# Optimization experiments

Hardware: AMD Instinct MI355X
Metric: run time of the kernel (lower is better)

Reference implementation:

```python
import jax, jax.numpy as jnp
import numpy as np
from jax import lax

B, h, Ch = 16, 8, 32
HW = 56
N = HW * HW
SPLITS = [64, 96, 96]  # [2*Ch, 3*Ch, 3*Ch] for windows {3,5,7}


def _dwconv(x, w, b, pad):
    # x: [B, C, H, W]; w: [C, 1, k, k] depthwise (feature_group_count=C)
    y = lax.conv_general_dilated(
        x, w, window_strides=(1, 1), padding=[(pad, pad), (pad, pad)],
        feature_group_count=x.shape[1],
        dimension_numbers=('NCHW', 'OIHW', 'NCHW'))
    return y + b[None, :, None, None]


def setup_inputs() -> dict:
    key = jax.random.key(0)
    ks = jax.random.split(key, 6)
    return {
        'q': jax.random.normal(ks[0], (B, h, N, Ch), dtype=jnp.float32),
        'v': jax.random.normal(ks[1], (B, h, N, Ch), dtype=jnp.float32),
        'w3': jax.random.normal(ks[2], (64, 1, 3, 3), dtype=jnp.float32) * 0.1,
        'b3': jnp.zeros((64,), dtype=jnp.float32),
        'w5': jax.random.normal(ks[3], (96, 1, 5, 5), dtype=jnp.float32) * 0.1,
        'b5': jnp.zeros((96,), dtype=jnp.float32),
        'w7': jax.random.normal(ks[4], (96, 1, 7, 7), dtype=jnp.float32) * 0.1,
        'b7': jnp.zeros((96,), dtype=jnp.float32),
        'H': HW,
        'W': HW,
    }


def reference(q, v, w3, b3, w5, b5, w7, b7, H, W):
    # q, v: [B, h, N, Ch]; N == H*W, Nv == N (same-resolution path, no interpolation)
    Bq, hh, Nq, C = q.shape
    # v: B h (H W) Ch -> B (h*Ch) H W
    v_img = jnp.transpose(v, (0, 1, 3, 2)).reshape(Bq, hh * C, H, W)
    v1, v2, v3 = jnp.split(v_img, np.cumsum(SPLITS)[:-1], axis=1)
    conv_v = jnp.concatenate([
        _dwconv(v1, w3, b3, 1),
        _dwconv(v2, w5, b5, 2),
        _dwconv(v3, w7, b7, 3),
    ], axis=1)  # [B, h*Ch, H, W]
    # B (h*Ch) H W -> B h (H W) Ch
    conv_v = conv_v.reshape(Bq, hh, C, H * W).transpose(0, 1, 3, 2)
    ev = q * conv_v  # [B, h, N, Ch]
    # transpose(1,2).flatten(2): [B, N, h*Ch]
    return jnp.transpose(ev, (0, 2, 1, 3)).reshape(Bq, Nq, hh * C)
```

## Files before the change

### kernel.cpp

```cpp
#include <hip/hip_runtime.h>
#include <cstddef>


#define BH 16
#define NH 8
#define CH 32
#define HW 56
#define NN (HW*HW)
#define ROWB (HW*CH*4)
#define BUF_PX 72
#define BUF_FLOATS (BUF_PX*CH)

typedef float f32x4 __attribute__((ext_vector_type(4)));
typedef unsigned int u32x4 __attribute__((ext_vector_type(4)));

__device__ __forceinline__ f32x4 bload(__amdgpu_buffer_rsrc_t rs, int voff) {
    u32x4 u = __builtin_amdgcn_raw_buffer_load_b128(rs, voff, 0, 0);
    f32x4 f; __builtin_memcpy(&f, &u, 16); return f;
}

template<int K>
__device__ __forceinline__ void run_head(
    const float* __restrict__ q, const float* __restrict__ v,
    const float* __restrict__ w, const float* __restrict__ bias,
    float* __restrict__ out, int b, int hh, int y0, int cbase,
    float* __restrict__ w_lds, float* __restrict__ bufs)
{
    constexpr int P = K / 2;
    constexpr int NR = 7 + K - 1;
    const int t = threadIdx.x;

    const int nw = K * K * CH;
    for (int i = t; i < nw; i += 256) {
        int tap = i >> 5, c = i & 31;
        w_lds[tap * CH + c] = w[(cbase + c) * (K * K) + tap];
    }
    __syncthreads();

    const int wid  = t >> 6;
    const int lane = t & 63;
    float* wb = bufs + wid * BUF_FLOATS;

    {
        f32x4 z = {0.f, 0.f, 0.f, 0.f};
        *(f32x4*)(wb + lane * 4) = z;
        *(f32x4*)(wb + 64 * CH + lane * 4) = z;
    }

    const int y    = y0 + wid;
    const int xseg = lane >> 3;
    const int chq  = lane & 7;
    const int x0   = xseg * 7;
    const int ch   = chq * 4;

    const size_t plane = ((size_t)b * NH + hh) * (size_t)NN * CH;
    const float* vb   = v + plane;
    const float* qrow = q + plane + (size_t)y * (HW * CH);

    f32x4 bias4 = *(const f32x4*)(bias + cbase + ch);
    f32x4 acc[7];
#pragma unroll
    for (int i = 0; i < 7; ++i) acc[i] = bias4;

#pragma unroll
    for (int dy = 0; dy < K; ++dy) {
        const int yy = y + dy - P;
        const bool ok = (unsigned)yy < (unsigned)HW;
        const float* base = vb + (ptrdiff_t)yy * (HW * CH);
        __amdgpu_buffer_rsrc_t rs = __builtin_amdgcn_make_buffer_rsrc(
            (void*)base, (short)0, ok ? ROWB : 0, 0x00020000);

        f32x4 ld[7];
#pragma unroll
        for (int k = 0; k < 7; ++k) ld[k] = bload(rs, k * 1024 + lane * 16);
#pragma unroll
        for (int k = 0; k < 7; ++k)
            *(f32x4*)(wb + (k + 1) * 256 + lane * 4) = ld[k];

        f32x4 r[NR];
        const float* rb = wb + (size_t)(x0 - P + 8) * CH + ch;
#pragma unroll
        for (int j = 0; j < NR; ++j)
            r[j] = *(const f32x4*)(rb + j * CH);

#pragma unroll
        for (int dx = 0; dx < K; ++dx) {
            const f32x4 w4 = *(const f32x4*)(w_lds + (dy * K + dx) * CH + ch);
#pragma unroll
            for (int i = 0; i < 7; ++i)
                acc[i] += r[i + dx] * w4;
        }
    }

#pragma unroll
    for (int i = 0; i < 7; ++i)
        *(f32x4*)(wb + (size_t)(x0 + i + 8) * CH + ch) = acc[i];

    float* orow = out + ((size_t)b * NN + (size_t)y * HW) * (NH * CH) + hh * CH;
    const int px_l = lane >> 3;
    const int chl  = (lane & 7) * 4;
#pragma unroll
    for (int k = 0; k < 7; ++k) {
        const f32x4 c4 = *(const f32x4*)(wb + (size_t)(k * 8 + px_l + 8) * CH + chl);
        const f32x4 q4 = *(const f32x4*)(qrow + k * 256 + lane * 4);
        const f32x4 o  = c4 * q4;
        *(f32x4*)(orow + (size_t)(k * 8 + px_l) * (NH * CH) + chl) = o;
    }
}

__global__ __launch_bounds__(256, 3)
void clusterformer_fused(const float* __restrict__ q, const float* __restrict__ v,
                         const float* __restrict__ w3, const float* __restrict__ b3,
                         const float* __restrict__ w5, const float* __restrict__ b5,
                         const float* __restrict__ w7, const float* __restrict__ b7,
                         float* __restrict__ out)
{
    __shared__ __align__(16) float bufs[4 * BUF_FLOATS];
    __shared__ __align__(16) float w_lds[49 * CH];

    const int bid  = blockIdx.x;
    const int p_lo = bid & 7;
    const int t2   = bid >> 3;
    const int p_hi = t2 / 14;
    const int yg   = t2 % 14;
    const int p    = p_hi * 8 + p_lo;
    const int b    = p & 15;
    const int hhp  = p >> 4;
    const int hh   = (hhp < 3) ? (5 + hhp) : ((hhp < 6) ? (hhp - 1) : (hhp - 6));
    const int y0   = yg * 4;

    if (hh < 2)      run_head<3>(q, v, w3, b3, out, b, hh, y0, hh * 32,       w_lds, bufs);
    else if (hh < 5) run_head<5>(q, v, w5, b5, out, b, hh, y0, hh * 32 - 64,  w_lds, bufs);
    else             run_head<7>(q, v, w7, b7, out, b, hh, y0, hh * 32 - 160, w_lds, bufs);
}

extern "C" void kernel_launch(void* const* d_in, const int* in_sizes, int n_in,
                              void* d_out, int out_size, void* d_ws, size_t ws_size,
                              hipStream_t stream) {
    const float* q  = (const float*)d_in[0];
    const float* v  = (const float*)d_in[1];
    const float* w3 = (const float*)d_in[2];
    const float* b3 = (const float*)d_in[3];
    const float* w5 = (const float*)d_in[4];
    const float* b5 = (const float*)d_in[5];
    const float* w7 = (const float*)d_in[6];
    const float* b7 = (const float*)d_in[7];
    float* out = (float*)d_out;

    const int grid = BH * NH * 14;
    clusterformer_fused<<<grid, 256, 0, stream>>>(q, v, w3, b3, w5, b5, w7, b7, out);
}
```

Baseline: 164.4 us.

## Load halo pixels directly from global via buffer loads, drop LDS staging

Instead of staging each input row through a per-wave LDS buffer and reading the shifted windows back out, each lane now issues buffer loads straight from global memory for all NR window pixels. Out-of-range columns get an out-of-bounds offset so the buffer hardware returns zeros. The output is written directly from registers rather than being transposed through LDS, and the occupancy hint rises from 3 to 4 blocks. This removes LDS traffic and frees LDS for occupancy, but issues more global loads (about NR/7 times as many, overlapping across lanes) and leaves the output stores less coalesced.

```diff
diff --git a/kernel.cpp b/kernel.cpp
--- a/kernel.cpp
+++ b/kernel.cpp
@@ -8,8 +8,6 @@
 #define HW 56
 #define NN (HW*HW)
 #define ROWB (HW*CH*4)
-#define BUF_PX 72
-#define BUF_FLOATS (BUF_PX*CH)
 
 typedef float f32x4 __attribute__((ext_vector_type(4)));
 typedef unsigned int u32x4 __attribute__((ext_vector_type(4)));
@@ -24,7 +22,7 @@
     const float* __restrict__ q, const float* __restrict__ v,
     const float* __restrict__ w, const float* __restrict__ bias,
     float* __restrict__ out, int b, int hh, int y0, int cbase,
-    float* __restrict__ w_lds, float* __restrict__ bufs)
+    float* __restrict__ w_lds)
 {
     constexpr int P = K / 2;
     constexpr int NR = 7 + K - 1;
@@ -39,14 +37,6 @@
 
     const int wid  = t >> 6;
     const int lane = t & 63;
-    float* wb = bufs + wid * BUF_FLOATS;
-
-    {
-        f32x4 z = {0.f, 0.f, 0.f, 0.f};
-        *(f32x4*)(wb + lane * 4) = z;
-        *(f32x4*)(wb + 64 * CH + lane * 4) = z;
-    }
-
     const int y    = y0 + wid;
     const int xseg = lane >> 3;
     const int chq  = lane & 7;
@@ -57,7 +47,14 @@
     const float* vb   = v + plane;
     const float* qrow = q + plane + (size_t)y * (HW * CH);
 
-    f32x4 bias4 = *(const f32x4*)(bias + cbase + ch);
+    int vx[NR];
+#pragma unroll
+    for (int j = 0; j < NR; ++j) {
+        const int px = x0 - P + j;
+        vx[j] = ((unsigned)px < (unsigned)HW) ? (px * CH + ch) * 4 : 0x40000000;
+    }
+
+    const f32x4 bias4 = *(const f32x4*)(bias + cbase + ch);
     f32x4 acc[7];
 #pragma unroll
     for (int i = 0; i < 7; ++i) acc[i] = bias4;
@@ -70,18 +67,9 @@
         __amdgpu_buffer_rsrc_t rs = __builtin_amdgcn_make_buffer_rsrc(
             (void*)base, (short)0, ok ? ROWB : 0, 0x00020000);
 
-        f32x4 ld[7];
+        f32x4 r[NR];
 #pragma unroll
-        for (int k = 0; k < 7; ++k) ld[k] = bload(rs, k * 1024 + lane * 16);
-#pragma unroll
-        for (int k = 0; k < 7; ++k)
-            *(f32x4*)(wb + (k + 1) * 256 + lane * 4) = ld[k];
-
-        f32x4 r[NR];
-        const float* rb = wb + (size_t)(x0 - P + 8) * CH + ch;
-#pragma unroll
-        for (int j = 0; j < NR; ++j)
-            r[j] = *(const f32x4*)(rb + j * CH);
+        for (int j = 0; j < NR; ++j) r[j] = bload(rs, vx[j]);
 
 #pragma unroll
         for (int dx = 0; dx < K; ++dx) {
@@ -92,30 +80,22 @@
         }
     }
 
+    float* obase = out + ((size_t)b * NN + (size_t)y * HW) * (NH * CH) + hh * CH + ch;
 #pragma unroll
-    for (int i = 0; i < 7; ++i)
-        *(f32x4*)(wb + (size_t)(x0 + i + 8) * CH + ch) = acc[i];
-
-    float* orow = out + ((size_t)b * NN + (size_t)y * HW) * (NH * CH) + hh * CH;
-    const int px_l = lane >> 3;
-    const int chl  = (lane & 7) * 4;
-#pragma unroll
-    for (int k = 0; k < 7; ++k) {
-        const f32x4 c4 = *(const f32x4*)(wb + (size_t)(k * 8 + px_l + 8) * CH + chl);
-        const f32x4 q4 = *(const f32x4*)(qrow + k * 256 + lane * 4);
-        const f32x4 o  = c4 * q4;
-        *(f32x4*)(orow + (size_t)(k * 8 + px_l) * (NH * CH) + chl) = o;
+    for (int i = 0; i < 7; ++i) {
+        const int px = x0 + i;
+        const f32x4 q4 = *(const f32x4*)(qrow + (size_t)px * CH + ch);
+        *(f32x4*)(obase + (size_t)px * (NH * CH)) = acc[i] * q4;
     }
 }
 
-__global__ __launch_bounds__(256, 3)
+__global__ __launch_bounds__(256, 4)
 void clusterformer_fused(const float* __restrict__ q, const float* __restrict__ v,
                          const float* __restrict__ w3, const float* __restrict__ b3,
                          const float* __restrict__ w5, const float* __restrict__ b5,
                          const float* __restrict__ w7, const float* __restrict__ b7,
                          float* __restrict__ out)
 {
-    __shared__ __align__(16) float bufs[4 * BUF_FLOATS];
     __shared__ __align__(16) float w_lds[49 * CH];
 
     const int bid  = blockIdx.x;
@@ -129,9 +109,9 @@
     const int hh   = (hhp < 3) ? (5 + hhp) : ((hhp < 6) ? (hhp - 1) : (hhp - 6));
     const int y0   = yg * 4;
 
-    if (hh < 2)      run_head<3>(q, v, w3, b3, out, b, hh, y0, hh * 32,       w_lds, bufs);
-    else if (hh < 5) run_head<5>(q, v, w5, b5, out, b, hh, y0, hh * 32 - 64,  w_lds, bufs);
-    else             run_head<7>(q, v, w7, b7, out, b, hh, y0, hh * 32 - 160, w_lds, bufs);
+    if (hh < 2)      run_head<3>(q, v, w3, b3, out, b, hh, y0, hh * 32,       w_lds);
+    else if (hh < 5) run_head<5>(q, v, w5, b5, out, b, hh, y0, hh * 32 - 64,  w_lds);
+    else             run_head<7>(q, v, w7, b7, out, b, hh, y0, hh * 32 - 160, w_lds);
 }
 
 extern "C" void kernel_launch(void* const* d_in, const int* in_sizes, int n_in,
```

New measurement: 167.6 us. No clear change (+2.0%).

## Share staged input row halo across waves in LDS instead of per-wave reloads

Applied to the files above, without the earlier changes.

The four waves of a block now cooperatively load the 4+2P input rows once into a single shared LDS tile with zero-padded borders. Previously each wave reloaded its own K rows from global memory, which duplicated traffic across the overlapping row halos. Q is preloaded into registers so the output is written directly, dropping the LDS round-trip used for the transpose. The cost is a larger LDS footprint, so launch bounds fall from 3 to 2 blocks per SM, and a block-wide barrier is added.

```diff
diff --git a/kernel.cpp b/kernel.cpp
--- a/kernel.cpp
+++ b/kernel.cpp
@@ -8,7 +8,8 @@
 #define HW 56
 #define NN (HW*HW)
 #define ROWB (HW*CH*4)
-#define BUF_PX 72
+#define RS 58
+#define BUF_PX 584
 #define BUF_FLOATS (BUF_PX*CH)
 
 typedef float f32x4 __attribute__((ext_vector_type(4)));
@@ -28,6 +29,7 @@
 {
     constexpr int P = K / 2;
     constexpr int NR = 7 + K - 1;
+    constexpr int NROWS = 4 + 2 * P;
     const int t = threadIdx.x;
 
     const int nw = K * K * CH;
@@ -35,18 +37,24 @@
         int tap = i >> 5, c = i & 31;
         w_lds[tap * CH + c] = w[(cbase + c) * (K * K) + tap];
     }
-    __syncthreads();
+
+    {
+        f32x4 z = {0.f, 0.f, 0.f, 0.f};
+        const int NG = P + 2 * NROWS + 1;
+        if (t < NG * 8) {
+            const int g = t >> 3, sub = t & 7;
+            int px;
+            if (g < P) px = g;
+            else if (g < P + 2 * NROWS) {
+                const int rr = (g - P) >> 1;
+                px = P + rr * RS + 56 + ((g - P) & 1);
+            } else px = P + NROWS * RS;
+            *(f32x4*)(bufs + px * CH + sub * 4) = z;
+        }
+    }
 
     const int wid  = t >> 6;
     const int lane = t & 63;
-    float* wb = bufs + wid * BUF_FLOATS;
-
-    {
-        f32x4 z = {0.f, 0.f, 0.f, 0.f};
-        *(f32x4*)(wb + lane * 4) = z;
-        *(f32x4*)(wb + 64 * CH + lane * 4) = z;
-    }
-
     const int y    = y0 + wid;
     const int xseg = lane >> 3;
     const int chq  = lane & 7;
@@ -57,31 +65,43 @@
     const float* vb   = v + plane;
     const float* qrow = q + plane + (size_t)y * (HW * CH);
 
-    f32x4 bias4 = *(const f32x4*)(bias + cbase + ch);
+    f32x4 qf[7];
+#pragma unroll
+    for (int i = 0; i < 7; ++i)
+        qf[i] = *(const f32x4*)(qrow + (size_t)(x0 + i) * CH + ch);
+
+    for (int rr = wid; rr < NROWS; rr += 4) {
+        const int yy = y0 - P + rr;
+        const bool ok = (unsigned)yy < (unsigned)HW;
+        __amdgpu_buffer_rsrc_t rs = __builtin_amdgcn_make_buffer_rsrc(
+            (void*)(vb + (ptrdiff_t)yy * (HW * CH)), (short)0, ok ? ROWB : 0, 0x00020000);
+        f32x4 ld[7];
+#pragma unroll
+        for (int k = 0; k < 7; ++k) ld[k] = bload(rs, k * 1024 + lane * 16);
+        float* dst = bufs + (size_t)(P + rr * RS) * CH;
+#pragma unroll
+        for (int k = 0; k < 7; ++k)
+            *(f32x4*)(dst + k * 256 + lane * 4) = ld[k];
+    }
+    __syncthreads();
+
+    const float mL = (xseg == 0) ? 0.f : 1.f;
+    const float mR = (xseg == 7) ? 0.f : 1.f;
+
+    const f32x4 bias4 = *(const f32x4*)(bias + cbase + ch);
     f32x4 acc[7];
 #pragma unroll
     for (int i = 0; i < 7; ++i) acc[i] = bias4;
 
 #pragma unroll
     for (int dy = 0; dy < K; ++dy) {
-        const int yy = y + dy - P;
-        const bool ok = (unsigned)yy < (unsigned)HW;
-        const float* base = vb + (ptrdiff_t)yy * (HW * CH);
-        __amdgpu_buffer_rsrc_t rs = __builtin_amdgcn_make_buffer_rsrc(
-            (void*)base, (short)0, ok ? ROWB : 0, 0x00020000);
-
-        f32x4 ld[7];
-#pragma unroll
-        for (int k = 0; k < 7; ++k) ld[k] = bload(rs, k * 1024 + lane * 16);
-#pragma unroll
-        for (int k = 0; k < 7; ++k)
-            *(f32x4*)(wb + (k + 1) * 256 + lane * 4) = ld[k];
-
+        const int rr = wid + dy;
+        const float* rb = bufs + (size_t)(rr * RS + x0) * CH + ch;
         f32x4 r[NR];
-        const float* rb = wb + (size_t)(x0 - P + 8) * CH + ch;
 #pragma unroll
         for (int j = 0; j < NR; ++j)
             r[j] = *(const f32x4*)(rb + j * CH);
+        if constexpr (K == 7) { r[0] *= mL; r[NR - 1] *= mR; }
 
 #pragma unroll
         for (int dx = 0; dx < K; ++dx) {
@@ -92,30 +112,20 @@
         }
     }
 
+    float* obase = out + ((size_t)b * NN + (size_t)y * HW) * (NH * CH) + hh * CH + ch;
 #pragma unroll
     for (int i = 0; i < 7; ++i)
-        *(f32x4*)(wb + (size_t)(x0 + i + 8) * CH + ch) = acc[i];
-
-    float* orow = out + ((size_t)b * NN + (size_t)y * HW) * (NH * CH) + hh * CH;
-    const int px_l = lane >> 3;
-    const int chl  = (lane & 7) * 4;
-#pragma unroll
-    for (int k = 0; k < 7; ++k) {
-        const f32x4 c4 = *(const f32x4*)(wb + (size_t)(k * 8 + px_l + 8) * CH + chl);
-        const f32x4 q4 = *(const f32x4*)(qrow + k * 256 + lane * 4);
-        const f32x4 o  = c4 * q4;
-        *(f32x4*)(orow + (size_t)(k * 8 + px_l) * (NH * CH) + chl) = o;
-    }
+        *(f32x4*)(obase + (size_t)(x0 + i) * (NH * CH)) = acc[i] * qf[i];
 }
 
-__global__ __launch_bounds__(256, 3)
+__global__ __launch_bounds__(256, 2)
 void clusterformer_fused(const float* __restrict__ q, const float* __restrict__ v,
                          const float* __restrict__ w3, const float* __restrict__ b3,
                          const float* __restrict__ w5, const float* __restrict__ b5,
                          const float* __restrict__ w7, const float* __restrict__ b7,
                          float* __restrict__ out)
 {
-    __shared__ __align__(16) float bufs[4 * BUF_FLOATS];
+    __shared__ __align__(16) float bufs[BUF_FLOATS];
     __shared__ __align__(16) float w_lds[49 * CH];
 
     const int bid  = blockIdx.x;
```

Result: no change. 161.8 us (-1.6%).

## Assign one output row across all heads per block and stage full-row output in LDS

Applied to the files above, without the earlier changes.

Each block now handles one (batch, row) pair across all 8 heads, with each wave processing two heads. Weights for all three kernel sizes are loaded into LDS once per block, and results are staged in an LDS row buffer so the global output write covers the full 256-channel row contiguously. The change also prefetches the next v row while the current one is processed (double-buffered registers) and loads q into registers early. The cost is a much larger LDS footprint (about 96KB) with launch bounds lowered to one block per CU, a grid of only 896 blocks, and unequal per-wave work, since waves pair 3x3, 5x5 and 7x7 heads differently.

```diff
diff --git a/kernel.cpp b/kernel.cpp
--- a/kernel.cpp
+++ b/kernel.cpp
@@ -8,8 +8,12 @@
 #define HW 56
 #define NN (HW*HW)
 #define ROWB (HW*CH*4)
-#define BUF_PX 72
-#define BUF_FLOATS (BUF_PX*CH)
+#define WBF 2304
+#define OUTROWF 264
+#define W3O 0
+#define W5O 576
+#define W7O 2976
+#define WTOT 7680
 
 typedef float f32x4 __attribute__((ext_vector_type(4)));
 typedef unsigned int u32x4 __attribute__((ext_vector_type(4)));
@@ -19,35 +23,16 @@
     f32x4 f; __builtin_memcpy(&f, &u, 16); return f;
 }
 
-template<int K>
-__device__ __forceinline__ void run_head(
+template<int K, int CT>
+__device__ __forceinline__ void head_row(
     const float* __restrict__ q, const float* __restrict__ v,
-    const float* __restrict__ w, const float* __restrict__ bias,
-    float* __restrict__ out, int b, int hh, int y0, int cbase,
-    float* __restrict__ w_lds, float* __restrict__ bufs)
+    const float* __restrict__ whead,
+    const float* __restrict__ bias_g,
+    float* __restrict__ outL, float* __restrict__ wb,
+    int b, int hh, int cbase, int y, int lane)
 {
-    constexpr int P = K / 2;
+    constexpr int P  = K / 2;
     constexpr int NR = 7 + K - 1;
-    const int t = threadIdx.x;
-
-    const int nw = K * K * CH;
-    for (int i = t; i < nw; i += 256) {
-        int tap = i >> 5, c = i & 31;
-        w_lds[tap * CH + c] = w[(cbase + c) * (K * K) + tap];
-    }
-    __syncthreads();
-
-    const int wid  = t >> 6;
-    const int lane = t & 63;
-    float* wb = bufs + wid * BUF_FLOATS;
-
-    {
-        f32x4 z = {0.f, 0.f, 0.f, 0.f};
-        *(f32x4*)(wb + lane * 4) = z;
-        *(f32x4*)(wb + 64 * CH + lane * 4) = z;
-    }
-
-    const int y    = y0 + wid;
     const int xseg = lane >> 3;
     const int chq  = lane & 7;
     const int x0   = xseg * 7;
@@ -56,36 +41,50 @@
     const size_t plane = ((size_t)b * NH + hh) * (size_t)NN * CH;
     const float* vb   = v + plane;
     const float* qrow = q + plane + (size_t)y * (HW * CH);
+    const float* whc  = whead + cbase + ch;
 
-    f32x4 bias4 = *(const f32x4*)(bias + cbase + ch);
+    f32x4 qf[7];
+#pragma unroll
+    for (int i = 0; i < 7; ++i)
+        qf[i] = *(const f32x4*)(qrow + (size_t)(x0 + i) * CH + ch);
+
+    const f32x4 bias4 = *(const f32x4*)(bias_g + ch);
     f32x4 acc[7];
 #pragma unroll
     for (int i = 0; i < 7; ++i) acc[i] = bias4;
 
+    f32x4 ld[2][7];
+    {
+        const int yy = y - P;
+        const bool ok = (unsigned)yy < (unsigned)HW;
+        __amdgpu_buffer_rsrc_t rs0 = __builtin_amdgcn_make_buffer_rsrc(
+            (void*)(vb + (ptrdiff_t)yy * (HW * CH)), (short)0, ok ? ROWB : 0, 0x00020000);
+#pragma unroll
+        for (int k = 0; k < 7; ++k) ld[0][k] = bload(rs0, k * 1024 + lane * 16);
+    }
 #pragma unroll
     for (int dy = 0; dy < K; ++dy) {
-        const int yy = y + dy - P;
-        const bool ok = (unsigned)yy < (unsigned)HW;
-        const float* base = vb + (ptrdiff_t)yy * (HW * CH);
-        __amdgpu_buffer_rsrc_t rs = __builtin_amdgcn_make_buffer_rsrc(
-            (void*)base, (short)0, ok ? ROWB : 0, 0x00020000);
-
-        f32x4 ld[7];
+        if (dy + 1 < K) {
+            const int yy = y + dy + 1 - P;
+            const bool ok = (unsigned)yy < (unsigned)HW;
+            __amdgpu_buffer_rsrc_t rs = __builtin_amdgcn_make_buffer_rsrc(
+                (void*)(vb + (ptrdiff_t)yy * (HW * CH)), (short)0, ok ? ROWB : 0, 0x00020000);
 #pragma unroll
-        for (int k = 0; k < 7; ++k) ld[k] = bload(rs, k * 1024 + lane * 16);
+            for (int k = 0; k < 7; ++k) ld[(dy + 1) & 1][k] = bload(rs, k * 1024 + lane * 16);
+        }
 #pragma unroll
         for (int k = 0; k < 7; ++k)
-            *(f32x4*)(wb + (k + 1) * 256 + lane * 4) = ld[k];
+            *(f32x4*)(wb + (k + 1) * 256 + lane * 4) = ld[dy & 1][k];
 
+        const float* rb = wb + (size_t)(x0 - P + 8) * CH + ch;
         f32x4 r[NR];
-        const float* rb = wb + (size_t)(x0 - P + 8) * CH + ch;
 #pragma unroll
         for (int j = 0; j < NR; ++j)
             r[j] = *(const f32x4*)(rb + j * CH);
 
 #pragma unroll
         for (int dx = 0; dx < K; ++dx) {
-            const f32x4 w4 = *(const f32x4*)(w_lds + (dy * K + dx) * CH + ch);
+            const f32x4 w4 = *(const f32x4*)(whc + (dy * K + dx) * CT);
 #pragma unroll
             for (int i = 0; i < 7; ++i)
                 acc[i] += r[i + dx] * w4;
@@ -94,44 +93,81 @@
 
 #pragma unroll
     for (int i = 0; i < 7; ++i)
-        *(f32x4*)(wb + (size_t)(x0 + i + 8) * CH + ch) = acc[i];
-
-    float* orow = out + ((size_t)b * NN + (size_t)y * HW) * (NH * CH) + hh * CH;
-    const int px_l = lane >> 3;
-    const int chl  = (lane & 7) * 4;
-#pragma unroll
-    for (int k = 0; k < 7; ++k) {
-        const f32x4 c4 = *(const f32x4*)(wb + (size_t)(k * 8 + px_l + 8) * CH + chl);
-        const f32x4 q4 = *(const f32x4*)(qrow + k * 256 + lane * 4);
-        const f32x4 o  = c4 * q4;
-        *(f32x4*)(orow + (size_t)(k * 8 + px_l) * (NH * CH) + chl) = o;
-    }
+        *(f32x4*)(outL + (size_t)(x0 + i) * OUTROWF + hh * CH + ch) = acc[i] * qf[i];
 }
 
-__global__ __launch_bounds__(256, 3)
+__device__ __forceinline__ void do_head(
+    const float* q, const float* v,
+    const float* w_lds,
+    const float* b3, const float* b5, const float* b7,
+    float* outL, float* wb, int b, int hh, int y, int lane)
+{
+    if (hh < 2)
+        head_row<3, 64>(q, v, w_lds + W3O, b3 + hh * 32,        outL, wb, b, hh, hh * 32,       y, lane);
+    else if (hh < 5)
+        head_row<5, 96>(q, v, w_lds + W5O, b5 + hh * 32 - 64,   outL, wb, b, hh, hh * 32 - 64,  y, lane);
+    else
+        head_row<7, 96>(q, v, w_lds + W7O, b7 + hh * 32 - 160,  outL, wb, b, hh, hh * 32 - 160, y, lane);
+}
+
+__global__ __launch_bounds__(256, 1)
 void clusterformer_fused(const float* __restrict__ q, const float* __restrict__ v,
                          const float* __restrict__ w3, const float* __restrict__ b3,
                          const float* __restrict__ w5, const float* __restrict__ b5,
                          const float* __restrict__ w7, const float* __restrict__ b7,
                          float* __restrict__ out)
 {
-    __shared__ __align__(16) float bufs[4 * BUF_FLOATS];
-    __shared__ __align__(16) float w_lds[49 * CH];
+    __shared__ __align__(16) float w_lds[WTOT];
+    __shared__ __align__(16) float bufs[4 * WBF];
+    __shared__ __align__(16) float outL[HW * OUTROWF];
+
+    const int t    = threadIdx.x;
+    const int wid  = t >> 6;
+    const int lane = t & 63;
 
     const int bid  = blockIdx.x;
-    const int p_lo = bid & 7;
-    const int t2   = bid >> 3;
-    const int p_hi = t2 / 14;
-    const int yg   = t2 % 14;
-    const int p    = p_hi * 8 + p_lo;
-    const int b    = p & 15;
-    const int hhp  = p >> 4;
-    const int hh   = (hhp < 3) ? (5 + hhp) : ((hhp < 6) ? (hhp - 1) : (hhp - 6));
-    const int y0   = yg * 4;
+    const int xcd  = bid & 7;
+    const int slot = bid >> 3;
+    const int b_hi = (slot >= 56) ? 1 : 0;
+    const int y    = slot - b_hi * 56;
+    const int b    = (b_hi << 3) | xcd;
 
-    if (hh < 2)      run_head<3>(q, v, w3, b3, out, b, hh, y0, hh * 32,       w_lds, bufs);
-    else if (hh < 5) run_head<5>(q, v, w5, b5, out, b, hh, y0, hh * 32 - 64,  w_lds, bufs);
-    else             run_head<7>(q, v, w7, b7, out, b, hh, y0, hh * 32 - 160, w_lds, bufs);
+    for (int i = t; i < WTOT; i += 256) {
+        float val;
+        if (i < W5O) {
+            const int tap = i >> 6, c = i & 63;
+            val = w3[c * 9 + tap];
+        } else if (i < W7O) {
+            const int j = i - W5O, tap = j / 96, c = j % 96;
+            val = w5[c * 25 + tap];
+        } else {
+            const int j = i - W7O, tap = j / 96, c = j % 96;
+            val = w7[c * 49 + tap];
+        }
+        w_lds[i] = val;
+    }
+
+    float* wb = bufs + wid * WBF;
+    {
+        f32x4 z = {0.f, 0.f, 0.f, 0.f};
+        *(f32x4*)(wb + lane * 4) = z;
+        *(f32x4*)(wb + 64 * CH + lane * 4) = z;
+    }
+    __syncthreads();
+
+    const int h2tab[4] = {5, 6, 7, 4};
+    do_head(q, v, w_lds, b3, b5, b7, outL, wb, b, wid,        y, lane);
+    do_head(q, v, w_lds, b3, b5, b7, outL, wb, b, h2tab[wid], y, lane);
+
+    __syncthreads();
+
+    float* orow = out + ((size_t)b * NN + (size_t)y * HW) * (NH * CH);
+#pragma unroll
+    for (int m = 0; m < 14; ++m) {
+        const int px = m * 4 + wid;
+        const f32x4 c4 = *(const f32x4*)(outL + (size_t)px * OUTROWF + lane * 4);
+        *(f32x4*)(orow + (size_t)px * (NH * CH) + lane * 4) = c4;
+    }
 }
 
 extern "C" void kernel_launch(void* const* d_in, const int* in_sizes, int n_in,
@@ -147,6 +183,6 @@
     const float* b7 = (const float*)d_in[7];
     float* out = (float*)d_out;
 
-    const int grid = BH * NH * 14;
+    const int grid = BH * HW;
     clusterformer_fused<<<grid, 256, 0, stream>>>(q, v, w3, b3, w5, b5, w7, b7, out);
 }
```

Measured after the change: 245.6 us. 1.49x slower.
